# Kernel optimization log

Hardware: AMD Instinct MI355X
Metric: run time of the kernel (lower is better)

The kernel has to match this reference:

```python
import jax, jax.numpy as jnp
import numpy as np

B, C_IN, T = 4, 256, 8192
LAYERS, STACKS = 24, 4
RES, GATE, SKIP, K = 128, 256, 128, 3
LPS = LAYERS // STACKS  # layers per stack -> dilation = 2**(i % LPS)
SQRT_HALF = 0.7071067811865476


def setup_inputs() -> dict:
    key = jax.random.key(0)
    ks = jax.random.split(key, 14)
    s = 0.08  # small init so the 24-layer stack stays well-scaled
    inp = {
        "x": jax.random.normal(ks[0], (B, C_IN, T), jnp.float32),
        "first_w": jax.random.normal(ks[1], (RES, C_IN), jnp.float32) * s,
        "first_b": jnp.zeros((RES,), jnp.float32),
        "conv_w": jax.random.normal(ks[2], (LAYERS, GATE, RES, K), jnp.float32) * s,
        "conv_b": jnp.zeros((LAYERS, GATE), jnp.float32),
        "out_w": jax.random.normal(ks[3], (LAYERS, RES, GATE // 2), jnp.float32) * s,
        "out_b": jnp.zeros((LAYERS, RES), jnp.float32),
        "skip_w": jax.random.normal(ks[4], (LAYERS, SKIP, GATE // 2), jnp.float32) * s,
        "skip_b": jnp.zeros((LAYERS, SKIP), jnp.float32),
        "last1_w": jax.random.normal(ks[5], (SKIP, SKIP), jnp.float32) * s,
        "last1_b": jnp.zeros((SKIP,), jnp.float32),
        "last2_w": jax.random.normal(ks[6], (C_IN, SKIP), jnp.float32) * s,
        "last2_b": jnp.zeros((C_IN,), jnp.float32),
    }
    return inp


def _conv1x1(w, b, h):
    # h: [B, C, T], w: [O, C]
    return jnp.einsum('oc,bct->bot', w, h) + b[None, :, None]


def _causal_dilated_conv(h, w, b, dilation):
    # left pad == torch symmetric pad (k-1)*d followed by crop to first T (causal)
    pad = (K - 1) * dilation
    hp = jnp.pad(h, ((0, 0), (0, 0), (pad, 0)))
    y = jax.lax.conv_general_dilated(
        hp, w, window_strides=(1,), padding='VALID',
        rhs_dilation=(dilation,), dimension_numbers=('NCH', 'OIH', 'NCH'))
    return y + b[None, :, None]


def reference(x, first_w, first_b, conv_w, conv_b, out_w, out_b,
              skip_w, skip_b, last1_w, last1_b, last2_w, last2_b):
    h = _conv1x1(first_w, first_b, x)  # [B, RES, T]
    skips = jnp.zeros((x.shape[0], SKIP, x.shape[-1]), h.dtype)
    for i in range(LAYERS):
        d = 2 ** (i % LPS)
        y = _causal_dilated_conv(h, conv_w[i], conv_b[i], d)  # [B, GATE, T]
        a, g = jnp.split(y, 2, axis=1)
        z = jnp.tanh(a) * jax.nn.sigmoid(g)  # gated tanh*sigmoid
        skips = skips + _conv1x1(skip_w[i], skip_b[i], z)
        h = (_conv1x1(out_w[i], out_b[i], z) + h) * SQRT_HALF  # residual
    skips = skips * (1.0 / LAYERS) ** 0.5
    out = jax.nn.relu(skips)
    out = jax.nn.relu(_conv1x1(last1_w, last1_b, out))
    out = _conv1x1(last2_w, last2_b, out)  # logits [B, 256, T]
    return out
```

## Files before the change

kernel.cpp:

```cpp
#include <hip/hip_runtime.h>

#define B 4
#define CIN 256
#define T 8192
#define NL 24
#define TP (64 + T + 8)
#define TT 64
#define SQRT_HALF 0.70710678118654752f
#define SKIP_SCALE 0.20412414523193150f

typedef unsigned short u16;
typedef __attribute__((ext_vector_type(4))) float f32x4;
typedef __attribute__((ext_vector_type(8))) short s16x8;
typedef __attribute__((ext_vector_type(4))) short s16x4;

__device__ inline u16 f2bf(float f) {
  unsigned u = __float_as_uint(f);
  return (u16)((u + 0x7fffu + ((u >> 16) & 1u)) >> 16);
}

__device__ inline void gload_lds16(const void* g, void* l) {
  __builtin_amdgcn_global_load_lds(
      (const __attribute__((address_space(1))) unsigned*)g,
      (__attribute__((address_space(3))) unsigned*)l, 16, 0, 0);
}

__device__ inline float gate_fn(float a, float g) {
  float e2 = __expf(-2.f * fabsf(a));
  float th = (1.f - e2) * __builtin_amdgcn_rcpf(1.f + e2);
  float sg = __builtin_amdgcn_rcpf(1.f + __expf(-g));
  return copysignf(th, a) * sg;
}

__global__ void cvt_convw(const float* __restrict__ src, u16* __restrict__ dst) {
  int i = blockIdx.x * 256 + threadIdx.x;
  if (i >= NL * 3 * 256 * 128) return;
  int c = i & 127, o = (i >> 7) & 255, kk = (i >> 15) % 3, l = (i >> 15) / 3;
  dst[i] = f2bf(src[(((size_t)l * 256 + o) * 128 + c) * 3 + kk]);
}
__global__ void cvt_sow(const float* __restrict__ skw, const float* __restrict__ otw,
                        u16* __restrict__ dst) {
  int i = blockIdx.x * 256 + threadIdx.x;
  if (i >= NL * 256 * 128) return;
  int c = i & 127, r = (i >> 7) & 255, l = i >> 15;
  float v = (r < 128) ? skw[((size_t)l * 128 + r) * 128 + c]
                      : otw[((size_t)l * 128 + (r - 128)) * 128 + c];
  dst[i] = f2bf(v);
}
__global__ void cvt_plain(const float* __restrict__ s, u16* __restrict__ d, int n) {
  int i = blockIdx.x * 256 + threadIdx.x;
  if (i < n) d[i] = f2bf(s[i]);
}
__global__ void padzero(u16* __restrict__ hb) {
  int i = blockIdx.x * 256 + threadIdx.x;
  if (i >= B * 64 * 128) return;
  int c = i & 127, r = (i >> 7) & 63, b = i >> 13;
  hb[((size_t)b * TP + r) * 128 + c] = 0;
}

__global__ __launch_bounds__(256, 2)
void first_kernel(const float* __restrict__ x, const u16* __restrict__ wf,
                  const float* __restrict__ fb, float* __restrict__ hf,
                  u16* __restrict__ hb) {
  __shared__ u16 xT[64 * 256];
  __shared__ u16 hoT[64 * 128];
  const int tid = threadIdx.x, wv = tid >> 6, lane = tid & 63, lo = lane & 15, hi = lane >> 4;
  const int t0 = blockIdx.x * 64, b = blockIdx.y;

  #pragma unroll
  for (int it = 0; it < 16; it++) {
    int idx = tid + it * 256;
    int c = idx >> 4, t4 = (idx & 15) << 2;
    f32x4 v = *(const f32x4*)(x + ((size_t)b * CIN + c) * T + t0 + t4);
    #pragma unroll
    for (int i = 0; i < 4; i++) {
      int t = t4 + i;
      *(u16*)((char*)xT + t * 512 + ((c * 2) ^ ((t & 7) << 4))) = f2bf(v[i]);
    }
  }
  __syncthreads();

  f32x4 acc[2][4];
  #pragma unroll
  for (int m = 0; m < 2; m++)
    #pragma unroll
    for (int n = 0; n < 4; n++) acc[m][n] = (f32x4){0.f, 0.f, 0.f, 0.f};

  #pragma unroll
  for (int s = 0; s < 8; s++) {
    s16x8 af[2], bf[4];
    #pragma unroll
    for (int m = 0; m < 2; m++)
      af[m] = *(const s16x8*)(wf + (size_t)(wv * 32 + m * 16 + lo) * CIN + s * 32 + hi * 8);
    #pragma unroll
    for (int n = 0; n < 4; n++) {
      int t = n * 16 + lo;
      bf[n] = *(const s16x8*)((const char*)xT + t * 512 + ((s * 64 + hi * 16) ^ ((t & 7) << 4)));
    }
    #pragma unroll
    for (int m = 0; m < 2; m++)
      #pragma unroll
      for (int n = 0; n < 4; n++)
        acc[m][n] = __builtin_amdgcn_mfma_f32_16x16x32_bf16(af[m], bf[n], acc[m][n], 0, 0, 0);
  }

  #pragma unroll
  for (int m = 0; m < 2; m++) {
    int c0 = wv * 32 + m * 16 + hi * 4;
    f32x4 bv = *(const f32x4*)(fb + c0);
    #pragma unroll
    for (int n = 0; n < 4; n++) {
      int t = n * 16 + lo;
      f32x4 h = acc[m][n] + bv;
      *(f32x4*)(hf + ((size_t)b * T + t0 + t) * 128 + c0) = h;
      s16x4 pk;
      #pragma unroll
      for (int j = 0; j < 4; j++) pk[j] = (short)f2bf(h[j]);
      *(s16x4*)((char*)hoT + t * 256 + ((c0 * 2) ^ ((t & 7) << 4))) = pk;
    }
  }
  __syncthreads();
  u16* gd = hb + ((size_t)b * TP + 64 + t0) * 128;
  #pragma unroll
  for (int i = 0; i < 4; i++)
    *(s16x8*)((char*)gd + (tid + i * 256) * 16) = *(const s16x8*)((const char*)hoT + (tid + i * 256) * 16);
}

__global__ __launch_bounds__(512, 4)
void layer_kernel(const u16* __restrict__ hbin, u16* __restrict__ hbout,
                  float* __restrict__ hf, float* __restrict__ skip,
                  const u16* __restrict__ wcv, const float* __restrict__ cb,
                  const u16* __restrict__ wso, const float* __restrict__ sb,
                  const float* __restrict__ ob, int d, int first) {
  __shared__ u16 h_s[128 * 128];
  __shared__ u16 zh[64 * 128];
  const int tid = threadIdx.x, wv = tid >> 6, lane = tid & 63, lo = lane & 15, hi = lane >> 4;
  const int t0 = blockIdx.x * TT, b = blockIdx.y;
  const int R = TT + 2 * d;
  const int nch = (R * 256 + 1023) >> 10;

  const char* src = (const char*)(hbin + ((size_t)b * TP + (64 + t0 - 2 * d)) * 128);
  for (int ch = wv; ch < nch; ch += 8)
    gload_lds16(src + ch * 1024 + lane * 16, (char*)h_s + ch * 1024);
  __syncthreads();

  f32x4 acc[2][4];
  #pragma unroll
  for (int m = 0; m < 2; m++)
    #pragma unroll
    for (int n = 0; n < 4; n++) acc[m][n] = (f32x4){0.f, 0.f, 0.f, 0.f};
  const int oa = wv * 16, og = 128 + wv * 16;

  #pragma unroll
  for (int k = 0; k < 3; k++) {
    const int jb = k * d;
    const int st = ((lo + (k + 6) * d) & 7) << 4;
    #pragma unroll
    for (int s = 0; s < 4; s++) {
      s16x8 af0 = *(const s16x8*)(wcv + ((size_t)(k * 256 + oa + lo)) * 128 + s * 32 + hi * 8);
      s16x8 af1 = *(const s16x8*)(wcv + ((size_t)(k * 256 + og + lo)) * 128 + s * 32 + hi * 8);
      const int cbyte = s * 64 + hi * 16;
      s16x8 bf[4];
      #pragma unroll
      for (int n = 0; n < 4; n++) {
        int j = n * 16 + lo + jb;
        bf[n] = *(const s16x8*)((const char*)h_s + j * 256 + (cbyte ^ st));
      }
      #pragma unroll
      for (int n = 0; n < 4; n++) {
        acc[0][n] = __builtin_amdgcn_mfma_f32_16x16x32_bf16(af0, bf[n], acc[0][n], 0, 0, 0);
        acc[1][n] = __builtin_amdgcn_mfma_f32_16x16x32_bf16(af1, bf[n], acc[1][n], 0, 0, 0);
      }
    }
  }

  {
    f32x4 ba = *(const f32x4*)(cb + oa + hi * 4);
    f32x4 bg = *(const f32x4*)(cb + og + hi * 4);
    #pragma unroll
    for (int n = 0; n < 4; n++) {
      int t = n * 16 + lo;
      s16x4 pk;
      #pragma unroll
      for (int j = 0; j < 4; j++)
        pk[j] = (short)f2bf(gate_fn(acc[0][n][j] + ba[j], acc[1][n][j] + bg[j]));
      *(s16x4*)((char*)zh + t * 256 + (((oa + hi * 4) * 2) ^ ((t & 7) << 4))) = pk;
    }
  }
  __syncthreads();

  #pragma unroll
  for (int m = 0; m < 2; m++)
    #pragma unroll
    for (int n = 0; n < 4; n++) acc[m][n] = (f32x4){0.f, 0.f, 0.f, 0.f};
  const int ro = wv * 32;
  #pragma unroll
  for (int s = 0; s < 4; s++) {
    s16x8 af0 = *(const s16x8*)(wso + (size_t)(ro + lo) * 128 + s * 32 + hi * 8);
    s16x8 af1 = *(const s16x8*)(wso + (size_t)(ro + 16 + lo) * 128 + s * 32 + hi * 8);
    const int cbyte = s * 64 + hi * 16;
    s16x8 bf[4];
    #pragma unroll
    for (int n = 0; n < 4; n++) {
      int t = n * 16 + lo;
      bf[n] = *(const s16x8*)((const char*)zh + t * 256 + (cbyte ^ ((t & 7) << 4)));
    }
    #pragma unroll
    for (int n = 0; n < 4; n++) {
      acc[0][n] = __builtin_amdgcn_mfma_f32_16x16x32_bf16(af0, bf[n], acc[0][n], 0, 0, 0);
      acc[1][n] = __builtin_amdgcn_mfma_f32_16x16x32_bf16(af1, bf[n], acc[1][n], 0, 0, 0);
    }
  }
  __syncthreads();

  if (wv < 4) {
    #pragma unroll
    for (int m = 0; m < 2; m++) {
      int c0 = wv * 32 + m * 16 + hi * 4;
      f32x4 sb4 = *(const f32x4*)(sb + c0);
      #pragma unroll
      for (int n = 0; n < 4; n++) {
        size_t off = ((size_t)b * T + t0 + n * 16 + lo) * 128 + c0;
        f32x4 r = acc[m][n] + sb4;
        if (!first) r += *(const f32x4*)(skip + off);
        *(f32x4*)(skip + off) = r;
      }
    }
  } else {
    #pragma unroll
    for (int m = 0; m < 2; m++) {
      int c0 = (wv - 4) * 32 + m * 16 + hi * 4;
      f32x4 ob4 = *(const f32x4*)(ob + c0);
      #pragma unroll
      for (int n = 0; n < 4; n++) {
        int tl = n * 16 + lo;
        size_t off = ((size_t)b * T + t0 + tl) * 128 + c0;
        f32x4 hn = (acc[m][n] + ob4 + *(const f32x4*)(hf + off)) * SQRT_HALF;
        *(f32x4*)(hf + off) = hn;
        s16x4 pk;
        #pragma unroll
        for (int j = 0; j < 4; j++) pk[j] = (short)f2bf(hn[j]);
        *(s16x4*)((char*)zh + tl * 256 + ((c0 * 2) ^ ((tl & 7) << 4))) = pk;
      }
    }
  }
  __syncthreads();
  u16* gd = hbout + ((size_t)b * TP + 64 + t0) * 128;
  #pragma unroll
  for (int i = 0; i < 2; i++)
    *(s16x8*)((char*)gd + (tid + i * 512) * 16) = *(const s16x8*)((const char*)zh + (tid + i * 512) * 16);
}

__global__ __launch_bounds__(256, 2)
void head1_kernel(const float* __restrict__ skip, const u16* __restrict__ w1,
                  const float* __restrict__ b1, u16* __restrict__ s1) {
  __shared__ u16 sT[64 * 128];
  const int tid = threadIdx.x, wv = tid >> 6, lane = tid & 63, lo = lane & 15, hi = lane >> 4;
  const int t0 = blockIdx.x * 64, b = blockIdx.y;

  #pragma unroll
  for (int it = 0; it < 8; it++) {
    int idx = tid + it * 256;
    int t = idx >> 5, c4 = idx & 31;
    f32x4 v = *(const f32x4*)(skip + ((size_t)b * T + t0 + t) * 128 + c4 * 4);
    s16x4 pk;
    #pragma unroll
    for (int i = 0; i < 4; i++) pk[i] = (short)f2bf(fmaxf(v[i] * SKIP_SCALE, 0.f));
    *(s16x4*)((char*)sT + t * 256 + ((c4 * 8) ^ ((t & 7) << 4))) = pk;
  }
  __syncthreads();

  f32x4 acc[2][4];
  #pragma unroll
  for (int m = 0; m < 2; m++)
    #pragma unroll
    for (int n = 0; n < 4; n++) acc[m][n] = (f32x4){0.f, 0.f, 0.f, 0.f};
  #pragma unroll
  for (int s = 0; s < 4; s++) {
    s16x8 af[2], bf[4];
    #pragma unroll
    for (int m = 0; m < 2; m++)
      af[m] = *(const s16x8*)(w1 + (size_t)(wv * 32 + m * 16 + lo) * 128 + s * 32 + hi * 8);
    #pragma unroll
    for (int n = 0; n < 4; n++) {
      int t = n * 16 + lo;
      bf[n] = *(const s16x8*)((const char*)sT + t * 256 + ((s * 64 + hi * 16) ^ ((t & 7) << 4)));
    }
    #pragma unroll
    for (int m = 0; m < 2; m++)
      #pragma unroll
      for (int n = 0; n < 4; n++)
        acc[m][n] = __builtin_amdgcn_mfma_f32_16x16x32_bf16(af[m], bf[n], acc[m][n], 0, 0, 0);
  }
  #pragma unroll
  for (int m = 0; m < 2; m++) {
    int c0 = wv * 32 + m * 16 + hi * 4;
    f32x4 bv = *(const f32x4*)(b1 + c0);
    #pragma unroll
    for (int n = 0; n < 4; n++) {
      int t = n * 16 + lo;
      s16x4 pk;
      #pragma unroll
      for (int j = 0; j < 4; j++) pk[j] = (short)f2bf(fmaxf(acc[m][n][j] + bv[j], 0.f));
      *(s16x4*)((char*)s1 + ((size_t)b * T + t0 + t) * 256 + ((c0 * 2) ^ ((t & 7) << 4))) = pk;
    }
  }
}

__global__ __launch_bounds__(256, 2)
void head2_kernel(const u16* __restrict__ s1, const u16* __restrict__ w2,
                  const float* __restrict__ b2, float* __restrict__ out) {
  __shared__ u16 s1T[64 * 128];
  const int tid = threadIdx.x, wv = tid >> 6, lane = tid & 63, lo = lane & 15, hi = lane >> 4;
  const int t0 = blockIdx.x * 64, b = blockIdx.y;

  const char* src = (const char*)(s1 + ((size_t)b * T + t0) * 128);
  #pragma unroll
  for (int i = 0; i < 4; i++)
    gload_lds16(src + (wv + i * 4) * 1024 + lane * 16, (char*)s1T + (wv + i * 4) * 1024);
  __syncthreads();

  f32x4 acc[4][4];
  #pragma unroll
  for (int m = 0; m < 4; m++)
    #pragma unroll
    for (int n = 0; n < 4; n++) acc[m][n] = (f32x4){0.f, 0.f, 0.f, 0.f};
  #pragma unroll
  for (int s = 0; s < 4; s++) {
    s16x8 af[4], bf[4];
    #pragma unroll
    for (int m = 0; m < 4; m++)
      af[m] = *(const s16x8*)(w2 + (size_t)(wv * 64 + m * 16 + lo) * 128 + s * 32 + hi * 8);
    #pragma unroll
    for (int n = 0; n < 4; n++) {
      int t = n * 16 + lo;
      bf[n] = *(const s16x8*)((const char*)s1T + t * 256 + ((s * 64 + hi * 16) ^ ((t & 7) << 4)));
    }
    #pragma unroll
    for (int m = 0; m < 4; m++)
      #pragma unroll
      for (int n = 0; n < 4; n++)
        acc[m][n] = __builtin_amdgcn_mfma_f32_16x16x32_bf16(af[m], bf[n], acc[m][n], 0, 0, 0);
  }
  #pragma unroll
  for (int m = 0; m < 4; m++) {
    int c0 = wv * 64 + m * 16 + hi * 4;
    f32x4 bv = *(const f32x4*)(b2 + c0);
    #pragma unroll
    for (int n = 0; n < 4; n++) {
      int t = t0 + n * 16 + lo;
      f32x4 r = acc[m][n] + bv;
      #pragma unroll
      for (int j = 0; j < 4; j++) out[((size_t)b * CIN + c0 + j) * T + t] = r[j];
    }
  }
}

extern "C" void kernel_launch(void* const* d_in, const int* in_sizes, int n_in,
                              void* d_out, int out_size, void* d_ws, size_t ws_size,
                              hipStream_t stream) {
  const float* x       = (const float*)d_in[0];
  const float* first_w = (const float*)d_in[1];
  const float* first_b = (const float*)d_in[2];
  const float* conv_w  = (const float*)d_in[3];
  const float* conv_b  = (const float*)d_in[4];
  const float* out_w   = (const float*)d_in[5];
  const float* out_b   = (const float*)d_in[6];
  const float* skip_w  = (const float*)d_in[7];
  const float* skip_b  = (const float*)d_in[8];
  const float* last1_w = (const float*)d_in[9];
  const float* last1_b = (const float*)d_in[10];
  const float* last2_w = (const float*)d_in[11];
  const float* last2_b = (const float*)d_in[12];
  float* out = (float*)d_out;

  u16* wsp  = (u16*)d_ws;
  u16* wcv  = wsp;
  u16* wsoB = wcv + (size_t)NL * 3 * 256 * 128;
  u16* wfB  = wsoB + (size_t)NL * 256 * 128;
  u16* w1B  = wfB + 128 * 256;
  u16* w2B  = w1B + 128 * 128;
  u16* hb0  = w2B + 256 * 128;
  u16* hb1  = hb0 + (size_t)B * TP * 128;
  u16* s1   = hb0;

  float* hf   = (float*)d_out;
  float* skip = hf + (size_t)B * T * 128;

  cvt_convw<<<NL * 3 * 256 * 128 / 256, 256, 0, stream>>>(conv_w, wcv);
  cvt_sow<<<NL * 256 * 128 / 256, 256, 0, stream>>>(skip_w, out_w, wsoB);
  cvt_plain<<<128, 256, 0, stream>>>(first_w, wfB, 128 * 256);
  cvt_plain<<<64, 256, 0, stream>>>(last1_w, w1B, 128 * 128);
  cvt_plain<<<128, 256, 0, stream>>>(last2_w, w2B, 256 * 128);
  padzero<<<128, 256, 0, stream>>>(hb0);
  padzero<<<128, 256, 0, stream>>>(hb1);

  dim3 g64(T / 64, B), gL(T / TT, B);
  first_kernel<<<g64, 256, 0, stream>>>(x, wfB, first_b, hf, hb0);
  for (int i = 0; i < NL; i++) {
    int d = 1 << (i % 6);
    layer_kernel<<<gL, 512, 0, stream>>>(
        (i & 1) ? hb1 : hb0, (i & 1) ? hb0 : hb1, hf, skip,
        wcv + (size_t)i * 3 * 256 * 128, conv_b + (size_t)i * 256,
        wsoB + (size_t)i * 256 * 128, skip_b + (size_t)i * 128,
        out_b + (size_t)i * 128, d, i == 0 ? 1 : 0);
  }
  head1_kernel<<<g64, 256, 0, stream>>>(skip, w1B, last1_b, s1);
  head2_kernel<<<g64, 256, 0, stream>>>(s1, w2B, last2_b, out);
}
```

Baseline: 759.2 us.

## Fuse whole WaveNet into one persistent kernel with neighbor flag synchronization

Replaces the first-conv kernel, 24 per-layer launches and two head kernels with a single persistent kernel of 512 blocks, one per 64-step time tile. Residual and skip accumulators stay in registers across layers, which removes the fp32 h and skip round trips through global memory. Only the bf16 halo is exchanged between neighbouring tiles, coordinated through per-block release/acquire flag and ack counters. Skip biases are pre-summed in a small kernel. The design relies on all 512 blocks being co-resident; if they are not, the spin-waits can deadlock, and they also serialise progress along the time axis.

```diff
diff --git a/kernel.cpp b/kernel.cpp
--- a/kernel.cpp
+++ b/kernel.cpp
@@ -5,7 +5,6 @@
 #define T 8192
 #define NL 24
 #define TP (64 + T + 8)
-#define TT 64
 #define SQRT_HALF 0.70710678118654752f
 #define SKIP_SCALE 0.20412414523193150f
 
@@ -18,13 +17,11 @@
   unsigned u = __float_as_uint(f);
   return (u16)((u + 0x7fffu + ((u >> 16) & 1u)) >> 16);
 }
-
 __device__ inline void gload_lds16(const void* g, void* l) {
   __builtin_amdgcn_global_load_lds(
       (const __attribute__((address_space(1))) unsigned*)g,
       (__attribute__((address_space(3))) unsigned*)l, 16, 0, 0);
 }
-
 __device__ inline float gate_fn(float a, float g) {
   float e2 = __expf(-2.f * fabsf(a));
   float th = (1.f - e2) * __builtin_amdgcn_rcpf(1.f + e2);
@@ -57,114 +54,67 @@
   int c = i & 127, r = (i >> 7) & 63, b = i >> 13;
   hb[((size_t)b * TP + r) * 128 + c] = 0;
 }
-
-__global__ __launch_bounds__(256, 2)
-void first_kernel(const float* __restrict__ x, const u16* __restrict__ wf,
-                  const float* __restrict__ fb, float* __restrict__ hf,
-                  u16* __restrict__ hb) {
-  __shared__ u16 xT[64 * 256];
-  __shared__ u16 hoT[64 * 128];
+__global__ void sumsb_kernel(const float* __restrict__ sb, float* __restrict__ dst) {
+  int c = threadIdx.x;
+  float s = 0.f;
+  for (int l = 0; l < NL; l++) s += sb[l * 128 + c];
+  dst[c] = s;
+}
+__global__ void zeroflags(int* __restrict__ f, int n) {
+  int i = blockIdx.x * 256 + threadIdx.x;
+  if (i < n) f[i] = 0;
+}
+
+__global__ __launch_bounds__(512, 4)
+void wavenet_kernel(const float* __restrict__ x,
+                    const u16* __restrict__ wf, const float* __restrict__ fb,
+                    const u16* __restrict__ wcv, const float* __restrict__ cbv,
+                    const u16* __restrict__ wso, const float* __restrict__ obv,
+                    const u16* __restrict__ w1, const float* __restrict__ b1,
+                    const u16* __restrict__ w2, const float* __restrict__ b2,
+                    const float* __restrict__ sumsb,
+                    u16* __restrict__ hG0, u16* __restrict__ hG1,
+                    int* __restrict__ flg, int* __restrict__ ack,
+                    float* __restrict__ out)
+{
+  __shared__ u16 h_s[128 * 128];
+  __shared__ u16 zh[64 * 128];
   const int tid = threadIdx.x, wv = tid >> 6, lane = tid & 63, lo = lane & 15, hi = lane >> 4;
-  const int t0 = blockIdx.x * 64, b = blockIdx.y;
-
-  #pragma unroll
-  for (int it = 0; it < 16; it++) {
-    int idx = tid + it * 256;
-    int c = idx >> 4, t4 = (idx & 15) << 2;
-    f32x4 v = *(const f32x4*)(x + ((size_t)b * CIN + c) * T + t0 + t4);
-    #pragma unroll
-    for (int i = 0; i < 4; i++) {
-      int t = t4 + i;
-      *(u16*)((char*)xT + t * 512 + ((c * 2) ^ ((t & 7) << 4))) = f2bf(v[i]);
-    }
-  }
-  __syncthreads();
-
+  const int bid = blockIdx.x, tj = bid & 127, b = bid >> 7, t0 = tj * 64;
+
+  f32x4 res[2][4];
   f32x4 acc[2][4];
   #pragma unroll
   for (int m = 0; m < 2; m++)
     #pragma unroll
-    for (int n = 0; n < 4; n++) acc[m][n] = (f32x4){0.f, 0.f, 0.f, 0.f};
+    for (int n = 0; n < 4; n++) res[m][n] = (f32x4){0.f, 0.f, 0.f, 0.f};
 
   #pragma unroll
-  for (int s = 0; s < 8; s++) {
-    s16x8 af[2], bf[4];
+  for (int it = 0; it < 8; it++) {
+    int idx = tid + it * 512;
+    int c = idx >> 4, t4 = (idx & 15) << 2;
+    f32x4 v = *(const f32x4*)(x + ((size_t)b * CIN + c) * T + t0 + t4);
+    #pragma unroll
+    for (int j = 0; j < 4; j++) {
+      int t = t4 + j;
+      *(u16*)((char*)h_s + t * 512 + ((c * 2) ^ ((t & 7) << 4))) = f2bf(v[j]);
+    }
+  }
+  __syncthreads();
+  if (wv >= 4) {
     #pragma unroll
     for (int m = 0; m < 2; m++)
-      af[m] = *(const s16x8*)(wf + (size_t)(wv * 32 + m * 16 + lo) * CIN + s * 32 + hi * 8);
-    #pragma unroll
-    for (int n = 0; n < 4; n++) {
-      int t = n * 16 + lo;
-      bf[n] = *(const s16x8*)((const char*)xT + t * 512 + ((s * 64 + hi * 16) ^ ((t & 7) << 4)));
-    }
-    #pragma unroll
-    for (int m = 0; m < 2; m++)
-      #pragma unroll
-      for (int n = 0; n < 4; n++)
-        acc[m][n] = __builtin_amdgcn_mfma_f32_16x16x32_bf16(af[m], bf[n], acc[m][n], 0, 0, 0);
-  }
-
-  #pragma unroll
-  for (int m = 0; m < 2; m++) {
-    int c0 = wv * 32 + m * 16 + hi * 4;
-    f32x4 bv = *(const f32x4*)(fb + c0);
-    #pragma unroll
-    for (int n = 0; n < 4; n++) {
-      int t = n * 16 + lo;
-      f32x4 h = acc[m][n] + bv;
-      *(f32x4*)(hf + ((size_t)b * T + t0 + t) * 128 + c0) = h;
-      s16x4 pk;
-      #pragma unroll
-      for (int j = 0; j < 4; j++) pk[j] = (short)f2bf(h[j]);
-      *(s16x4*)((char*)hoT + t * 256 + ((c0 * 2) ^ ((t & 7) << 4))) = pk;
-    }
-  }
-  __syncthreads();
-  u16* gd = hb + ((size_t)b * TP + 64 + t0) * 128;
-  #pragma unroll
-  for (int i = 0; i < 4; i++)
-    *(s16x8*)((char*)gd + (tid + i * 256) * 16) = *(const s16x8*)((const char*)hoT + (tid + i * 256) * 16);
-}
-
-__global__ __launch_bounds__(512, 4)
-void layer_kernel(const u16* __restrict__ hbin, u16* __restrict__ hbout,
-                  float* __restrict__ hf, float* __restrict__ skip,
-                  const u16* __restrict__ wcv, const float* __restrict__ cb,
-                  const u16* __restrict__ wso, const float* __restrict__ sb,
-                  const float* __restrict__ ob, int d, int first) {
-  __shared__ u16 h_s[128 * 128];
-  __shared__ u16 zh[64 * 128];
-  const int tid = threadIdx.x, wv = tid >> 6, lane = tid & 63, lo = lane & 15, hi = lane >> 4;
-  const int t0 = blockIdx.x * TT, b = blockIdx.y;
-  const int R = TT + 2 * d;
-  const int nch = (R * 256 + 1023) >> 10;
-
-  const char* src = (const char*)(hbin + ((size_t)b * TP + (64 + t0 - 2 * d)) * 128);
-  for (int ch = wv; ch < nch; ch += 8)
-    gload_lds16(src + ch * 1024 + lane * 16, (char*)h_s + ch * 1024);
-  __syncthreads();
-
-  f32x4 acc[2][4];
-  #pragma unroll
-  for (int m = 0; m < 2; m++)
-    #pragma unroll
-    for (int n = 0; n < 4; n++) acc[m][n] = (f32x4){0.f, 0.f, 0.f, 0.f};
-  const int oa = wv * 16, og = 128 + wv * 16;
-
-  #pragma unroll
-  for (int k = 0; k < 3; k++) {
-    const int jb = k * d;
-    const int st = ((lo + (k + 6) * d) & 7) << 4;
-    #pragma unroll
-    for (int s = 0; s < 4; s++) {
-      s16x8 af0 = *(const s16x8*)(wcv + ((size_t)(k * 256 + oa + lo)) * 128 + s * 32 + hi * 8);
-      s16x8 af1 = *(const s16x8*)(wcv + ((size_t)(k * 256 + og + lo)) * 128 + s * 32 + hi * 8);
-      const int cbyte = s * 64 + hi * 16;
+      #pragma unroll
+      for (int n = 0; n < 4; n++) acc[m][n] = (f32x4){0.f, 0.f, 0.f, 0.f};
+    #pragma unroll
+    for (int s = 0; s < 8; s++) {
+      s16x8 af0 = *(const s16x8*)(wf + (size_t)((wv - 4) * 32 + lo) * CIN + s * 32 + hi * 8);
+      s16x8 af1 = *(const s16x8*)(wf + (size_t)((wv - 4) * 32 + 16 + lo) * CIN + s * 32 + hi * 8);
       s16x8 bf[4];
       #pragma unroll
       for (int n = 0; n < 4; n++) {
-        int j = n * 16 + lo + jb;
-        bf[n] = *(const s16x8*)((const char*)h_s + j * 256 + (cbyte ^ st));
+        int t = n * 16 + lo;
+        bf[n] = *(const s16x8*)((const char*)h_s + t * 512 + ((s * 64 + hi * 16) ^ ((t & 7) << 4)));
       }
       #pragma unroll
       for (int n = 0; n < 4; n++) {
@@ -172,186 +122,267 @@
         acc[1][n] = __builtin_amdgcn_mfma_f32_16x16x32_bf16(af1, bf[n], acc[1][n], 0, 0, 0);
       }
     }
-  }
-
+    #pragma unroll
+    for (int m = 0; m < 2; m++) {
+      f32x4 fb4 = *(const f32x4*)(fb + (wv - 4) * 32 + m * 16 + hi * 4);
+      #pragma unroll
+      for (int n = 0; n < 4; n++) res[m][n] = acc[m][n] + fb4;
+    }
+    #pragma unroll
+    for (int m = 0; m < 2; m++) {
+      int c0 = (wv - 4) * 32 + m * 16 + hi * 4;
+      #pragma unroll
+      for (int n = 0; n < 4; n++) {
+        int tl = n * 16 + lo;
+        s16x4 pk;
+        #pragma unroll
+        for (int j = 0; j < 4; j++) pk[j] = (short)f2bf(res[m][n][j]);
+        *(s16x4*)((char*)zh + tl * 256 + ((c0 * 2) ^ ((tl & 7) << 4))) = pk;
+      }
+    }
+  }
+  __syncthreads();
   {
-    f32x4 ba = *(const f32x4*)(cb + oa + hi * 4);
-    f32x4 bg = *(const f32x4*)(cb + og + hi * 4);
-    #pragma unroll
-    for (int n = 0; n < 4; n++) {
-      int t = n * 16 + lo;
-      s16x4 pk;
-      #pragma unroll
-      for (int j = 0; j < 4; j++)
-        pk[j] = (short)f2bf(gate_fn(acc[0][n][j] + ba[j], acc[1][n][j] + bg[j]));
-      *(s16x4*)((char*)zh + t * 256 + (((oa + hi * 4) * 2) ^ ((t & 7) << 4))) = pk;
-    }
+    u16* gd = hG0 + ((size_t)b * TP + 64 + t0) * 128;
+    #pragma unroll
+    for (int i = 0; i < 2; i++)
+      *(s16x8*)((char*)gd + (tid + i * 512) * 16) = *(const s16x8*)((const char*)zh + (tid + i * 512) * 16);
   }
   __syncthreads();
-
-  #pragma unroll
-  for (int m = 0; m < 2; m++)
-    #pragma unroll
-    for (int n = 0; n < 4; n++) acc[m][n] = (f32x4){0.f, 0.f, 0.f, 0.f};
-  const int ro = wv * 32;
-  #pragma unroll
-  for (int s = 0; s < 4; s++) {
-    s16x8 af0 = *(const s16x8*)(wso + (size_t)(ro + lo) * 128 + s * 32 + hi * 8);
-    s16x8 af1 = *(const s16x8*)(wso + (size_t)(ro + 16 + lo) * 128 + s * 32 + hi * 8);
-    const int cbyte = s * 64 + hi * 16;
-    s16x8 bf[4];
-    #pragma unroll
-    for (int n = 0; n < 4; n++) {
-      int t = n * 16 + lo;
-      bf[n] = *(const s16x8*)((const char*)zh + t * 256 + (cbyte ^ ((t & 7) << 4)));
-    }
-    #pragma unroll
-    for (int n = 0; n < 4; n++) {
-      acc[0][n] = __builtin_amdgcn_mfma_f32_16x16x32_bf16(af0, bf[n], acc[0][n], 0, 0, 0);
-      acc[1][n] = __builtin_amdgcn_mfma_f32_16x16x32_bf16(af1, bf[n], acc[1][n], 0, 0, 0);
-    }
-  }
-  __syncthreads();
+  if (tid == 0)
+    __hip_atomic_store(flg + bid * 32, 1, __ATOMIC_RELEASE, __HIP_MEMORY_SCOPE_AGENT);
+
+  #pragma unroll 1
+  for (int i = 0; i < NL; i++) {
+    const int d = 1 << (i % 6);
+    const u16* hGin = (i & 1) ? hG1 : hG0;
+    const u16* wc = wcv + (size_t)i * 3 * 256 * 128;
+    const float* cb = cbv + i * 256;
+    const u16* wsl = wso + (size_t)i * 256 * 128;
+    const float* ob = obv + i * 128;
+
+    if (wv >= 4) {
+      #pragma unroll
+      for (int m = 0; m < 2; m++) {
+        int c0 = (wv - 4) * 32 + m * 16 + hi * 4;
+        #pragma unroll
+        for (int n = 0; n < 4; n++) {
+          int tl = n * 16 + lo;
+          s16x4 pk;
+          #pragma unroll
+          for (int j = 0; j < 4; j++) pk[j] = (short)f2bf(res[m][n][j]);
+          *(s16x4*)((char*)h_s + (2 * d + tl) * 256 + ((c0 * 2) ^ ((tl & 7) << 4))) = pk;
+        }
+      }
+    } else if (tid == 0 && tj > 0) {
+      while (__hip_atomic_load(flg + (bid - 1) * 32, __ATOMIC_ACQUIRE, __HIP_MEMORY_SCOPE_AGENT) < i + 1)
+        __builtin_amdgcn_s_sleep(1);
+    }
+    __syncthreads();
+    if (wv < 4) {
+      const char* src = (const char*)(hGin + ((size_t)b * TP + 64 + t0 - 2 * d) * 128);
+      int q = wv * 64 + lane;
+      for (int p = q; p < 32 * d; p += 256)
+        gload_lds16(src + p * 16, (char*)h_s + p * 16);
+    }
+    __syncthreads();
+    if (tid == 0)
+      __hip_atomic_store(ack + bid * 32, i + 1, __ATOMIC_RELEASE, __HIP_MEMORY_SCOPE_AGENT);
+
+    #pragma unroll
+    for (int m = 0; m < 2; m++)
+      #pragma unroll
+      for (int n = 0; n < 4; n++) acc[m][n] = (f32x4){0.f, 0.f, 0.f, 0.f};
+    const int oa = wv * 16, og = 128 + wv * 16;
+    #pragma unroll
+    for (int k = 0; k < 3; k++) {
+      const int jb = k * d;
+      const int st = ((lo + (k + 6) * d) & 7) << 4;
+      #pragma unroll
+      for (int s = 0; s < 4; s++) {
+        s16x8 af0 = *(const s16x8*)(wc + ((size_t)(k * 256 + oa + lo)) * 128 + s * 32 + hi * 8);
+        s16x8 af1 = *(const s16x8*)(wc + ((size_t)(k * 256 + og + lo)) * 128 + s * 32 + hi * 8);
+        const int cbyte = s * 64 + hi * 16;
+        s16x8 bf[4];
+        #pragma unroll
+        for (int n = 0; n < 4; n++) {
+          int j = n * 16 + lo + jb;
+          bf[n] = *(const s16x8*)((const char*)h_s + j * 256 + (cbyte ^ st));
+        }
+        #pragma unroll
+        for (int n = 0; n < 4; n++) {
+          acc[0][n] = __builtin_amdgcn_mfma_f32_16x16x32_bf16(af0, bf[n], acc[0][n], 0, 0, 0);
+          acc[1][n] = __builtin_amdgcn_mfma_f32_16x16x32_bf16(af1, bf[n], acc[1][n], 0, 0, 0);
+        }
+      }
+    }
+    {
+      f32x4 ba = *(const f32x4*)(cb + oa + hi * 4);
+      f32x4 bg = *(const f32x4*)(cb + og + hi * 4);
+      #pragma unroll
+      for (int n = 0; n < 4; n++) {
+        int tl = n * 16 + lo;
+        s16x4 pk;
+        #pragma unroll
+        for (int j = 0; j < 4; j++)
+          pk[j] = (short)f2bf(gate_fn(acc[0][n][j] + ba[j], acc[1][n][j] + bg[j]));
+        *(s16x4*)((char*)zh + tl * 256 + (((oa + hi * 4) * 2) ^ ((tl & 7) << 4))) = pk;
+      }
+    }
+    __syncthreads();
+
+    const int ro = wv * 32;
+    if (wv < 4) {
+      #pragma unroll
+      for (int s = 0; s < 4; s++) {
+        s16x8 af0 = *(const s16x8*)(wsl + (size_t)(ro + lo) * 128 + s * 32 + hi * 8);
+        s16x8 af1 = *(const s16x8*)(wsl + (size_t)(ro + 16 + lo) * 128 + s * 32 + hi * 8);
+        const int cbyte = s * 64 + hi * 16;
+        s16x8 bf[4];
+        #pragma unroll
+        for (int n = 0; n < 4; n++) {
+          int tl = n * 16 + lo;
+          bf[n] = *(const s16x8*)((const char*)zh + tl * 256 + (cbyte ^ ((tl & 7) << 4)));
+        }
+        #pragma unroll
+        for (int n = 0; n < 4; n++) {
+          res[0][n] = __builtin_amdgcn_mfma_f32_16x16x32_bf16(af0, bf[n], res[0][n], 0, 0, 0);
+          res[1][n] = __builtin_amdgcn_mfma_f32_16x16x32_bf16(af1, bf[n], res[1][n], 0, 0, 0);
+        }
+      }
+    } else {
+      #pragma unroll
+      for (int m = 0; m < 2; m++)
+        #pragma unroll
+        for (int n = 0; n < 4; n++) acc[m][n] = (f32x4){0.f, 0.f, 0.f, 0.f};
+      #pragma unroll
+      for (int s = 0; s < 4; s++) {
+        s16x8 af0 = *(const s16x8*)(wsl + (size_t)(ro + lo) * 128 + s * 32 + hi * 8);
+        s16x8 af1 = *(const s16x8*)(wsl + (size_t)(ro + 16 + lo) * 128 + s * 32 + hi * 8);
+        const int cbyte = s * 64 + hi * 16;
+        s16x8 bf[4];
+        #pragma unroll
+        for (int n = 0; n < 4; n++) {
+          int tl = n * 16 + lo;
+          bf[n] = *(const s16x8*)((const char*)zh + tl * 256 + (cbyte ^ ((tl & 7) << 4)));
+        }
+        #pragma unroll
+        for (int n = 0; n < 4; n++) {
+          acc[0][n] = __builtin_amdgcn_mfma_f32_16x16x32_bf16(af0, bf[n], acc[0][n], 0, 0, 0);
+          acc[1][n] = __builtin_amdgcn_mfma_f32_16x16x32_bf16(af1, bf[n], acc[1][n], 0, 0, 0);
+        }
+      }
+      #pragma unroll
+      for (int m = 0; m < 2; m++) {
+        f32x4 ob4 = *(const f32x4*)(ob + (ro - 128) + m * 16 + hi * 4);
+        #pragma unroll
+        for (int n = 0; n < 4; n++)
+          res[m][n] = (acc[m][n] + ob4 + res[m][n]) * SQRT_HALF;
+      }
+    }
+    __syncthreads();
+
+    if (i < NL - 1) {
+      if (wv >= 4) {
+        #pragma unroll
+        for (int m = 0; m < 2; m++) {
+          int c0 = (wv - 4) * 32 + m * 16 + hi * 4;
+          #pragma unroll
+          for (int n = 0; n < 4; n++) {
+            int tl = n * 16 + lo;
+            s16x4 pk;
+            #pragma unroll
+            for (int j = 0; j < 4; j++) pk[j] = (short)f2bf(res[m][n][j]);
+            *(s16x4*)((char*)zh + tl * 256 + ((c0 * 2) ^ ((tl & 7) << 4))) = pk;
+          }
+        }
+      } else if (tid == 0 && tj < 127) {
+        while (__hip_atomic_load(ack + (bid + 1) * 32, __ATOMIC_ACQUIRE, __HIP_MEMORY_SCOPE_AGENT) < i)
+          __builtin_amdgcn_s_sleep(1);
+      }
+      __syncthreads();
+      u16* gd = ((i & 1) ? hG0 : hG1) + ((size_t)b * TP + 64 + t0) * 128;
+      #pragma unroll
+      for (int q2 = 0; q2 < 2; q2++)
+        *(s16x8*)((char*)gd + (tid + q2 * 512) * 16) = *(const s16x8*)((const char*)zh + (tid + q2 * 512) * 16);
+      __syncthreads();
+      if (tid == 0)
+        __hip_atomic_store(flg + bid * 32, i + 2, __ATOMIC_RELEASE, __HIP_MEMORY_SCOPE_AGENT);
+    }
+  }
 
   if (wv < 4) {
     #pragma unroll
     for (int m = 0; m < 2; m++) {
       int c0 = wv * 32 + m * 16 + hi * 4;
-      f32x4 sb4 = *(const f32x4*)(sb + c0);
-      #pragma unroll
-      for (int n = 0; n < 4; n++) {
-        size_t off = ((size_t)b * T + t0 + n * 16 + lo) * 128 + c0;
-        f32x4 r = acc[m][n] + sb4;
-        if (!first) r += *(const f32x4*)(skip + off);
-        *(f32x4*)(skip + off) = r;
-      }
-    }
-  } else {
+      f32x4 sv = *(const f32x4*)(sumsb + c0);
+      #pragma unroll
+      for (int n = 0; n < 4; n++) {
+        int tl = n * 16 + lo;
+        s16x4 pk;
+        #pragma unroll
+        for (int j = 0; j < 4; j++)
+          pk[j] = (short)f2bf(fmaxf((res[m][n][j] + sv[j]) * SKIP_SCALE, 0.f));
+        *(s16x4*)((char*)h_s + tl * 256 + ((c0 * 2) ^ ((tl & 7) << 4))) = pk;
+      }
+    }
+  }
+  __syncthreads();
+  {
+    f32x4 a1[4];
+    #pragma unroll
+    for (int n = 0; n < 4; n++) a1[n] = (f32x4){0.f, 0.f, 0.f, 0.f};
+    #pragma unroll
+    for (int s = 0; s < 4; s++) {
+      s16x8 af = *(const s16x8*)(w1 + (size_t)(wv * 16 + lo) * 128 + s * 32 + hi * 8);
+      #pragma unroll
+      for (int n = 0; n < 4; n++) {
+        int tl = n * 16 + lo;
+        s16x8 bf = *(const s16x8*)((const char*)h_s + tl * 256 + ((s * 64 + hi * 16) ^ ((tl & 7) << 4)));
+        a1[n] = __builtin_amdgcn_mfma_f32_16x16x32_bf16(af, bf, a1[n], 0, 0, 0);
+      }
+    }
+    int c0 = wv * 16 + hi * 4;
+    f32x4 b14 = *(const f32x4*)(b1 + c0);
+    #pragma unroll
+    for (int n = 0; n < 4; n++) {
+      int tl = n * 16 + lo;
+      s16x4 pk;
+      #pragma unroll
+      for (int j = 0; j < 4; j++) pk[j] = (short)f2bf(fmaxf(a1[n][j] + b14[j], 0.f));
+      *(s16x4*)((char*)zh + tl * 256 + ((c0 * 2) ^ ((tl & 7) << 4))) = pk;
+    }
+  }
+  __syncthreads();
+  {
+    const int ro = wv * 32;
+    #pragma unroll
+    for (int m = 0; m < 2; m++)
+      #pragma unroll
+      for (int n = 0; n < 4; n++) acc[m][n] = (f32x4){0.f, 0.f, 0.f, 0.f};
+    #pragma unroll
+    for (int s = 0; s < 4; s++) {
+      s16x8 af0 = *(const s16x8*)(w2 + (size_t)(ro + lo) * 128 + s * 32 + hi * 8);
+      s16x8 af1 = *(const s16x8*)(w2 + (size_t)(ro + 16 + lo) * 128 + s * 32 + hi * 8);
+      #pragma unroll
+      for (int n = 0; n < 4; n++) {
+        int tl = n * 16 + lo;
+        s16x8 bf = *(const s16x8*)((const char*)zh + tl * 256 + ((s * 64 + hi * 16) ^ ((tl & 7) << 4)));
+        acc[0][n] = __builtin_amdgcn_mfma_f32_16x16x32_bf16(af0, bf, acc[0][n], 0, 0, 0);
+        acc[1][n] = __builtin_amdgcn_mfma_f32_16x16x32_bf16(af1, bf, acc[1][n], 0, 0, 0);
+      }
+    }
     #pragma unroll
     for (int m = 0; m < 2; m++) {
-      int c0 = (wv - 4) * 32 + m * 16 + hi * 4;
-      f32x4 ob4 = *(const f32x4*)(ob + c0);
-      #pragma unroll
-      for (int n = 0; n < 4; n++) {
-        int tl = n * 16 + lo;
-        size_t off = ((size_t)b * T + t0 + tl) * 128 + c0;
-        f32x4 hn = (acc[m][n] + ob4 + *(const f32x4*)(hf + off)) * SQRT_HALF;
-        *(f32x4*)(hf + off) = hn;
-        s16x4 pk;
-        #pragma unroll
-        for (int j = 0; j < 4; j++) pk[j] = (short)f2bf(hn[j]);
-        *(s16x4*)((char*)zh + tl * 256 + ((c0 * 2) ^ ((tl & 7) << 4))) = pk;
-      }
-    }
-  }
-  __syncthreads();
-  u16* gd = hbout + ((size_t)b * TP + 64 + t0) * 128;
-  #pragma unroll
-  for (int i = 0; i < 2; i++)
-    *(s16x8*)((char*)gd + (tid + i * 512) * 16) = *(const s16x8*)((const char*)zh + (tid + i * 512) * 16);
-}
-
-__global__ __launch_bounds__(256, 2)
-void head1_kernel(const float* __restrict__ skip, const u16* __restrict__ w1,
-                  const float* __restrict__ b1, u16* __restrict__ s1) {
-  __shared__ u16 sT[64 * 128];
-  const int tid = threadIdx.x, wv = tid >> 6, lane = tid & 63, lo = lane & 15, hi = lane >> 4;
-  const int t0 = blockIdx.x * 64, b = blockIdx.y;
-
-  #pragma unroll
-  for (int it = 0; it < 8; it++) {
-    int idx = tid + it * 256;
-    int t = idx >> 5, c4 = idx & 31;
-    f32x4 v = *(const f32x4*)(skip + ((size_t)b * T + t0 + t) * 128 + c4 * 4);
-    s16x4 pk;
-    #pragma unroll
-    for (int i = 0; i < 4; i++) pk[i] = (short)f2bf(fmaxf(v[i] * SKIP_SCALE, 0.f));
-    *(s16x4*)((char*)sT + t * 256 + ((c4 * 8) ^ ((t & 7) << 4))) = pk;
-  }
-  __syncthreads();
-
-  f32x4 acc[2][4];
-  #pragma unroll
-  for (int m = 0; m < 2; m++)
-    #pragma unroll
-    for (int n = 0; n < 4; n++) acc[m][n] = (f32x4){0.f, 0.f, 0.f, 0.f};
-  #pragma unroll
-  for (int s = 0; s < 4; s++) {
-    s16x8 af[2], bf[4];
-    #pragma unroll
-    for (int m = 0; m < 2; m++)
-      af[m] = *(const s16x8*)(w1 + (size_t)(wv * 32 + m * 16 + lo) * 128 + s * 32 + hi * 8);
-    #pragma unroll
-    for (int n = 0; n < 4; n++) {
-      int t = n * 16 + lo;
-      bf[n] = *(const s16x8*)((const char*)sT + t * 256 + ((s * 64 + hi * 16) ^ ((t & 7) << 4)));
-    }
-    #pragma unroll
-    for (int m = 0; m < 2; m++)
-      #pragma unroll
-      for (int n = 0; n < 4; n++)
-        acc[m][n] = __builtin_amdgcn_mfma_f32_16x16x32_bf16(af[m], bf[n], acc[m][n], 0, 0, 0);
-  }
-  #pragma unroll
-  for (int m = 0; m < 2; m++) {
-    int c0 = wv * 32 + m * 16 + hi * 4;
-    f32x4 bv = *(const f32x4*)(b1 + c0);
-    #pragma unroll
-    for (int n = 0; n < 4; n++) {
-      int t = n * 16 + lo;
-      s16x4 pk;
-      #pragma unroll
-      for (int j = 0; j < 4; j++) pk[j] = (short)f2bf(fmaxf(acc[m][n][j] + bv[j], 0.f));
-      *(s16x4*)((char*)s1 + ((size_t)b * T + t0 + t) * 256 + ((c0 * 2) ^ ((t & 7) << 4))) = pk;
-    }
-  }
-}
-
-__global__ __launch_bounds__(256, 2)
-void head2_kernel(const u16* __restrict__ s1, const u16* __restrict__ w2,
-                  const float* __restrict__ b2, float* __restrict__ out) {
-  __shared__ u16 s1T[64 * 128];
-  const int tid = threadIdx.x, wv = tid >> 6, lane = tid & 63, lo = lane & 15, hi = lane >> 4;
-  const int t0 = blockIdx.x * 64, b = blockIdx.y;
-
-  const char* src = (const char*)(s1 + ((size_t)b * T + t0) * 128);
-  #pragma unroll
-  for (int i = 0; i < 4; i++)
-    gload_lds16(src + (wv + i * 4) * 1024 + lane * 16, (char*)s1T + (wv + i * 4) * 1024);
-  __syncthreads();
-
-  f32x4 acc[4][4];
-  #pragma unroll
-  for (int m = 0; m < 4; m++)
-    #pragma unroll
-    for (int n = 0; n < 4; n++) acc[m][n] = (f32x4){0.f, 0.f, 0.f, 0.f};
-  #pragma unroll
-  for (int s = 0; s < 4; s++) {
-    s16x8 af[4], bf[4];
-    #pragma unroll
-    for (int m = 0; m < 4; m++)
-      af[m] = *(const s16x8*)(w2 + (size_t)(wv * 64 + m * 16 + lo) * 128 + s * 32 + hi * 8);
-    #pragma unroll
-    for (int n = 0; n < 4; n++) {
-      int t = n * 16 + lo;
-      bf[n] = *(const s16x8*)((const char*)s1T + t * 256 + ((s * 64 + hi * 16) ^ ((t & 7) << 4)));
-    }
-    #pragma unroll
-    for (int m = 0; m < 4; m++)
-      #pragma unroll
-      for (int n = 0; n < 4; n++)
-        acc[m][n] = __builtin_amdgcn_mfma_f32_16x16x32_bf16(af[m], bf[n], acc[m][n], 0, 0, 0);
-  }
-  #pragma unroll
-  for (int m = 0; m < 4; m++) {
-    int c0 = wv * 64 + m * 16 + hi * 4;
-    f32x4 bv = *(const f32x4*)(b2 + c0);
-    #pragma unroll
-    for (int n = 0; n < 4; n++) {
-      int t = t0 + n * 16 + lo;
-      f32x4 r = acc[m][n] + bv;
-      #pragma unroll
-      for (int j = 0; j < 4; j++) out[((size_t)b * CIN + c0 + j) * T + t] = r[j];
+      int c0 = ro + m * 16 + hi * 4;
+      f32x4 b24 = *(const f32x4*)(b2 + c0);
+      #pragma unroll
+      for (int n = 0; n < 4; n++) {
+        int t = t0 + n * 16 + lo;
+        #pragma unroll
+        for (int j = 0; j < 4; j++)
+          out[((size_t)b * CIN + c0 + j) * T + t] = acc[m][n][j] + b24[j];
+      }
     }
   }
 }
@@ -374,37 +405,29 @@
   const float* last2_b = (const float*)d_in[12];
   float* out = (float*)d_out;
 
-  u16* wsp  = (u16*)d_ws;
-  u16* wcv  = wsp;
+  u16* wsp = (u16*)d_ws;
+  u16* wcv = wsp;
   u16* wsoB = wcv + (size_t)NL * 3 * 256 * 128;
-  u16* wfB  = wsoB + (size_t)NL * 256 * 128;
-  u16* w1B  = wfB + 128 * 256;
-  u16* w2B  = w1B + 128 * 128;
-  u16* hb0  = w2B + 256 * 128;
-  u16* hb1  = hb0 + (size_t)B * TP * 128;
-  u16* s1   = hb0;
-
-  float* hf   = (float*)d_out;
-  float* skip = hf + (size_t)B * T * 128;
+  u16* wfB = wsoB + (size_t)NL * 256 * 128;
+  u16* w1B = wfB + 128 * 256;
+  u16* w2B = w1B + 128 * 128;
+  float* sumsb = (float*)(w2B + 256 * 128);
+  u16* hG0 = (u16*)(sumsb + 128);
+  u16* hG1 = hG0 + (size_t)B * TP * 128;
+  int* flg = (int*)(hG1 + (size_t)B * TP * 128);
+  int* ack = flg + 512 * 32;
 
   cvt_convw<<<NL * 3 * 256 * 128 / 256, 256, 0, stream>>>(conv_w, wcv);
   cvt_sow<<<NL * 256 * 128 / 256, 256, 0, stream>>>(skip_w, out_w, wsoB);
   cvt_plain<<<128, 256, 0, stream>>>(first_w, wfB, 128 * 256);
   cvt_plain<<<64, 256, 0, stream>>>(last1_w, w1B, 128 * 128);
   cvt_plain<<<128, 256, 0, stream>>>(last2_w, w2B, 256 * 128);
-  padzero<<<128, 256, 0, stream>>>(hb0);
-  padzero<<<128, 256, 0, stream>>>(hb1);
-
-  dim3 g64(T / 64, B), gL(T / TT, B);
-  first_kernel<<<g64, 256, 0, stream>>>(x, wfB, first_b, hf, hb0);
-  for (int i = 0; i < NL; i++) {
-    int d = 1 << (i % 6);
-    layer_kernel<<<gL, 512, 0, stream>>>(
-        (i & 1) ? hb1 : hb0, (i & 1) ? hb0 : hb1, hf, skip,
-        wcv + (size_t)i * 3 * 256 * 128, conv_b + (size_t)i * 256,
-        wsoB + (size_t)i * 256 * 128, skip_b + (size_t)i * 128,
-        out_b + (size_t)i * 128, d, i == 0 ? 1 : 0);
-  }
-  head1_kernel<<<g64, 256, 0, stream>>>(skip, w1B, last1_b, s1);
-  head2_kernel<<<g64, 256, 0, stream>>>(s1, w2B, last2_b, out);
-}
+  sumsb_kernel<<<1, 128, 0, stream>>>(skip_b, sumsb);
+  padzero<<<128, 256, 0, stream>>>(hG0);
+  padzero<<<128, 256, 0, stream>>>(hG1);
+  zeroflags<<<128, 256, 0, stream>>>(flg, 512 * 32 * 2);
+
+  wavenet_kernel<<<dim3(512), dim3(512), 0, stream>>>(
+      x, wfB, first_b, wcv, conv_b, wsoB, out_b, w1B, last1_b, w2B, last2_b,
+      sumsb, hG0, hG1, flg, ack, out);
+}
```

Result: slower. 1.258 ms (+65.7%).
